# Kernel optimization log

Hardware: AMD Instinct MI355X
Metric: run time of the kernel (lower is better)

## Reference

```python
import jax, jax.numpy as jnp
import numpy as np

B, T, D = 8, 2048, 1024

def _ln(x, g, b, eps=1e-5):
    mu = x.mean(-1, keepdims=True)
    var = ((x - mu) ** 2).mean(-1, keepdims=True)
    return (x - mu) * jax.lax.rsqrt(var + eps) * g + b

def setup_inputs() -> dict:
    key = jax.random.key(0)
    ks = jax.random.split(key, 8)
    s = 1.0 / np.sqrt(D)
    return {
        "x": jax.random.normal(ks[0], (B, T, D), jnp.float32),
        "Wq": jax.random.normal(ks[1], (D, D), jnp.float32) * s,
        "bq": jnp.zeros((D,), jnp.float32),
        "Wk": jax.random.normal(ks[2], (D, D), jnp.float32) * s,
        "bk": jnp.zeros((D,), jnp.float32),
        "Wv": jax.random.normal(ks[3], (D, D), jnp.float32) * s,
        "bv": jnp.zeros((D,), jnp.float32),
        "pos_bias": jax.random.normal(ks[4], (T, T), jnp.float32) * 0.1,
        "ln1_g": jnp.ones((D,), jnp.float32),
        "ln1_b": jnp.zeros((D,), jnp.float32),
        "W1": jax.random.normal(ks[5], (D, 4 * D), jnp.float32) * s,
        "b1": jnp.zeros((4 * D,), jnp.float32),
        "W2": jax.random.normal(ks[6], (4 * D, D), jnp.float32) * (1.0 / np.sqrt(4 * D)),
        "b2": jnp.zeros((D,), jnp.float32),
        "ln2_g": jnp.ones((D,), jnp.float32),
        "ln2_b": jnp.zeros((D,), jnp.float32),
    }

def reference(x, Wq, bq, Wk, bk, Wv, bv, pos_bias, ln1_g, ln1_b,
              W1, b1, W2, b2, ln2_g, ln2_b):
    # --- pre-norm AFT-full attention + residual ---
    h = _ln(x, ln1_g, ln1_b)
    q = h @ Wq + bq                      # [B,T,D]
    k = h @ Wk + bk
    v = h @ Wv + bv
    # global-max stabilization (cancels in the ratio)
    ek = jnp.exp(k - jax.lax.stop_gradient(k.max()))
    ew = jnp.exp(pos_bias - jax.lax.stop_gradient(pos_bias.max()))  # [T,T]
    num = jnp.einsum('ts,bsd->btd', ew, ek * v)
    den = jnp.einsum('ts,bsd->btd', ew, ek)
    attn = jax.nn.sigmoid(q) * (num / den)
    x = attn + x
    # --- pre-norm MLP + residual ---
    h = _ln(x, ln2_g, ln2_b)
    h = jax.nn.relu(h @ W1 + b1) @ W2 + b2
    return h + x
```

## Files before the change

### kernel.cpp

```cpp
#include <hip/hip_runtime.h>
#include <hip/hip_bf16.h>
#include <stdint.h>

typedef __hip_bfloat16 bf16;
typedef __attribute__((ext_vector_type(4))) float f32x4;
typedef __attribute__((ext_vector_type(8))) short bf16x8;

#define BB   8
#define TT   2048
#define DD   1024
#define MM   (BB * TT)

enum { EPI_Q = 0, EPI_K, EPI_V, EPI_ND, EPI_MLP1, EPI_MLP2 };

static __device__ __forceinline__ void async_ld16(const bf16* g, bf16* l) {
  __builtin_amdgcn_global_load_lds(
      (const __attribute__((address_space(1))) void*)g,
      (__attribute__((address_space(3))) void*)l, 16, 0, 0);
}

template<int EPI>
__global__ __launch_bounds__(512, 2)
void gemm_bt(const bf16* __restrict__ A, const bf16* __restrict__ B,
             int M, int N, int K,
             long long strideAz, long long strideBz,
             float* __restrict__ Cf,
             bf16* __restrict__ Cb, long long strideCz,
             const float* __restrict__ bias,
             const float* __restrict__ add,
             bf16* __restrict__ ekv)
{
  (void)M;
  __shared__ __align__(16) bf16 lds[65536];

  const int tid  = threadIdx.x;
  const int wave = tid >> 6;
  const int lane = tid & 63;

  const int nwg = (int)gridDim.x;
  const int bid = (int)blockIdx.x;
  const int swz = (bid & 7) * (nwg >> 3) + (bid >> 3);
  int bn, bm, bz;
  if constexpr (EPI == EPI_ND) {
    bn = swz & 7; bm = (swz >> 3) & 7; bz = swz >> 6;
  } else {
    const int nbn = N >> 8;
    const int lnb = 31 - __clz(nbn);
    bn = swz & (nbn - 1); bm = swz >> lnb; bz = 0;
  }
  A += (size_t)bz * strideAz;
  B += (size_t)bz * strideBz;

  const int wm = (wave >> 2) * 128;
  const int wn = (wave & 3) * 64;

  const int lr = lane >> 2;
  const int lc = (((lane & 3) ^ ((lane >> 3) & 3))) * 8;
  const bf16* Ag0 = A + ((size_t)bm * 256 + wave * 32 + lr) * K + lc;
  const bf16* Bg0 = B + ((size_t)bn * 256 + wave * 32 + lr) * K + lc;
  const size_t K16 = (size_t)16 * K;
  const int ldsAW = wave * 1024;
  const int ldsBW = 32768 + wave * 1024;
  const int NT = K >> 5;

  auto stageA = [&](int tt) {
    const int bo = (tt & 3) * 8192;
    const bf16* g = Ag0 + (size_t)(tt & (NT - 1)) * 32;
    async_ld16(g,       &lds[bo + ldsAW]);
    async_ld16(g + K16, &lds[bo + ldsAW + 512]);
  };
  auto stageB = [&](int tt) {
    const int bo = (tt & 3) * 8192;
    const bf16* g = Bg0 + (size_t)(tt & (NT - 1)) * 32;
    async_ld16(g,       &lds[bo + ldsBW]);
    async_ld16(g + K16, &lds[bo + ldsBW + 512]);
  };

  f32x4 acc[8][4];
#pragma unroll
  for (int i = 0; i < 8; ++i)
#pragma unroll
    for (int j = 0; j < 4; ++j) acc[i][j] = {0.f, 0.f, 0.f, 0.f};

  stageA(0); stageB(0);
  stageA(1); stageB(1);
  stageA(2); stageB(2);
  __builtin_amdgcn_sched_barrier(0);
  asm volatile("s_waitcnt vmcnt(8)" ::: "memory");
  __builtin_amdgcn_s_barrier();
  __builtin_amdgcn_sched_barrier(0);

  const int fm32 = (lane & 15) * 32;
  const int qs = (((lane >> 4) ^ ((lane >> 1) & 3))) * 8;

  bf16x8 bfrP[4], bfrN[4], afA[4], afB[4];

  {
    const int ab0 = wm * 32 + fm32 + qs;
    const int bb0 = 32768 + wn * 32 + fm32 + qs;
#pragma unroll
    for (int j = 0; j < 4; ++j) bfrP[j] = *(const bf16x8*)&lds[bb0 + j * 512];
#pragma unroll
    for (int i = 0; i < 4; ++i) afA[i] = *(const bf16x8*)&lds[ab0 + i * 512];
  }
  __builtin_amdgcn_sched_barrier(0);

#define TILE_BODY(t, bfrC, bfrX)                                               \
  {                                                                            \
    const int ab  = ((t) & 3) * 8192 + wm * 32 + fm32 + qs;                    \
    const int abn = (((t) + 1) & 3) * 8192 + wm * 32 + fm32 + qs;              \
    const int bbn = 32768 + (((t) + 1) & 3) * 8192 + wn * 32 + fm32 + qs;      \
                                                        \
    _Pragma("unroll")                                                          \
    for (int i = 0; i < 4; ++i)                                                \
      afB[i] = *(const bf16x8*)&lds[ab + 2048 + i * 512];                      \
    stageA((t) + 3);                                                           \
    __builtin_amdgcn_sched_barrier(0);                                         \
    asm volatile("s_waitcnt vmcnt(6) lgkmcnt(4)" ::: "memory");                \
    __builtin_amdgcn_sched_barrier(0);                                         \
    __builtin_amdgcn_s_setprio(1);                                             \
    _Pragma("unroll")                                                          \
    for (int i = 0; i < 4; ++i)                                                \
      _Pragma("unroll")                                                        \
      for (int j = 0; j < 4; ++j)                                              \
        acc[i][j] = __builtin_amdgcn_mfma_f32_16x16x32_bf16(                   \
            afA[i], bfrC[j], acc[i][j], 0, 0, 0);                              \
    __builtin_amdgcn_s_setprio(0);                                             \
    __builtin_amdgcn_s_barrier();                                              \
    __builtin_amdgcn_sched_barrier(0);                                         \
                                                        \
    _Pragma("unroll")                                                          \
    for (int j = 0; j < 4; ++j)                                                \
      bfrX[j] = *(const bf16x8*)&lds[bbn + j * 512];                           \
    _Pragma("unroll")                                                          \
    for (int i = 0; i < 4; ++i)                                                \
      afA[i] = *(const bf16x8*)&lds[abn + i * 512];                            \
    stageB((t) + 3);                                                           \
    __builtin_amdgcn_sched_barrier(0);                                         \
    asm volatile("s_waitcnt lgkmcnt(8)" ::: "memory");                         \
    __builtin_amdgcn_sched_barrier(0);                                         \
    __builtin_amdgcn_s_setprio(1);                                             \
    _Pragma("unroll")                                                          \
    for (int i = 0; i < 4; ++i)                                                \
      _Pragma("unroll")                                                        \
      for (int j = 0; j < 4; ++j)                                              \
        acc[4 + i][j] = __builtin_amdgcn_mfma_f32_16x16x32_bf16(               \
            afB[i], bfrC[j], acc[4 + i][j], 0, 0, 0);                          \
    __builtin_amdgcn_s_setprio(0);                                             \
    __builtin_amdgcn_s_barrier();                                              \
    __builtin_amdgcn_sched_barrier(0);                                         \
  }

  for (int tp = 0; tp < NT; tp += 2) {
    TILE_BODY(tp,     bfrP, bfrN);
    TILE_BODY(tp + 1, bfrN, bfrP);
  }
#undef TILE_BODY

  const int cr = (lane >> 4) * 4;
  const int cc = lane & 15;
#pragma unroll
  for (int i = 0; i < 8; ++i) {
#pragma unroll
    for (int j = 0; j < 4; ++j) {
#pragma unroll
      for (int r = 0; r < 4; ++r) {
        const int gm = bm * 256 + wm + i * 16 + cr + r;
        const int gn = bn * 256 + wn + j * 16 + cc;
        float v = acc[i][j][r];
        if constexpr (EPI == EPI_Q) {
          v += bias[gn];
          Cb[(size_t)gm * N + gn] = __float2bfloat16(v);
        } else if constexpr (EPI == EPI_K) {
          v = __expf(v + bias[gm]);
          const int b = gn >> 11, t = gn & (TT - 1);
          ekv[((size_t)b << 22) + (size_t)(1024 + gm) * TT + t] =
              __float2bfloat16(v);
        } else if constexpr (EPI == EPI_V) {
          v += bias[gm];
          const int b = gn >> 11, t = gn & (TT - 1);
          const size_t base = ((size_t)b << 22);
          const float ek =
              __bfloat162float(ekv[base + (size_t)(1024 + gm) * TT + t]);
          ekv[base + (size_t)gm * TT + t] = __float2bfloat16(v * ek);
        } else if constexpr (EPI == EPI_ND) {
          Cb[(size_t)bz * strideCz + (size_t)gm * N + gn] =
              __float2bfloat16(v);
        } else if constexpr (EPI == EPI_MLP1) {
          v = fmaxf(v + bias[gn], 0.0f);
          Cb[(size_t)gm * N + gn] = __float2bfloat16(v);
        } else {
          v += bias[gn] + add[(size_t)gm * N + gn];
          Cf[(size_t)gm * N + gn] = v;
        }
      }
    }
  }
}

__global__ __launch_bounds__(256)
void transpose_cast(const float* __restrict__ W, bf16* __restrict__ Wt,
                    int K, int N)
{
  __shared__ float tile[32][33];
  const int n0 = blockIdx.x * 32, k0 = blockIdx.y * 32;
  const int tx = threadIdx.x, ty = threadIdx.y;
#pragma unroll
  for (int i = 0; i < 32; i += 8)
    tile[ty + i][tx] = W[(size_t)(k0 + ty + i) * N + n0 + tx];
  __syncthreads();
#pragma unroll
  for (int i = 0; i < 32; i += 8)
    Wt[(size_t)(n0 + ty + i) * K + k0 + tx] =
        __float2bfloat16(tile[tx][ty + i]);
}

__global__ __launch_bounds__(256)
void ew_kernel(const float* __restrict__ pb, bf16* __restrict__ ew)
{
  const size_t gid = (size_t)blockIdx.x * 256 + threadIdx.x;
  const float4 v = *(const float4*)(pb + gid * 4);
  union { bf16 h[4]; unsigned long long u; } pk;
  pk.h[0] = __float2bfloat16(__expf(v.x));
  pk.h[1] = __float2bfloat16(__expf(v.y));
  pk.h[2] = __float2bfloat16(__expf(v.z));
  pk.h[3] = __float2bfloat16(__expf(v.w));
  *(unsigned long long*)(ew + gid * 4) = pk.u;
}

__global__ __launch_bounds__(256)
void ln_kernel(const float* __restrict__ x, const float* __restrict__ g,
               const float* __restrict__ b, bf16* __restrict__ out)
{
  const int row = blockIdx.x;
  const int tid = threadIdx.x;
  const float4 v = ((const float4*)(x + (size_t)row * DD))[tid];
  float s  = v.x + v.y + v.z + v.w;
  float s2 = v.x * v.x + v.y * v.y + v.z * v.z + v.w * v.w;
#pragma unroll
  for (int o = 32; o; o >>= 1) {
    s  += __shfl_down(s, o);
    s2 += __shfl_down(s2, o);
  }
  __shared__ float red[8];
  if ((tid & 63) == 0) { red[tid >> 6] = s; red[4 + (tid >> 6)] = s2; }
  __syncthreads();
  const float ts  = red[0] + red[1] + red[2] + red[3];
  const float ts2 = red[4] + red[5] + red[6] + red[7];
  const float mu = ts * (1.0f / DD);
  const float rs = rsqrtf(ts2 * (1.0f / DD) - mu * mu + 1e-5f);
  const float4 gv = ((const float4*)g)[tid];
  const float4 bv = ((const float4*)b)[tid];
  union { bf16 h[4]; unsigned long long u; } pk;
  pk.h[0] = __float2bfloat16((v.x - mu) * rs * gv.x + bv.x);
  pk.h[1] = __float2bfloat16((v.y - mu) * rs * gv.y + bv.y);
  pk.h[2] = __float2bfloat16((v.z - mu) * rs * gv.z + bv.z);
  pk.h[3] = __float2bfloat16((v.w - mu) * rs * gv.w + bv.w);
  ((unsigned long long*)(out + (size_t)row * DD))[tid] = pk.u;
}

__global__ __launch_bounds__(256)
void combine_ln_kernel(const bf16* __restrict__ q, const bf16* __restrict__ nd,
                       const float* __restrict__ x,
                       const float* __restrict__ g, const float* __restrict__ b,
                       float* __restrict__ x2, bf16* __restrict__ hout)
{
  const int row = blockIdx.x;
  const int tid = threadIdx.x;
  const int c = tid * 4;
  const bf16* ndr = nd + (size_t)row * 2048;
  union { unsigned long long u; bf16 h[4]; } un, ud, uq;
  un.u = *(const unsigned long long*)(ndr + c);
  ud.u = *(const unsigned long long*)(ndr + 1024 + c);
  uq.u = *(const unsigned long long*)(q + (size_t)row * DD + c);
  const float4 xv = *(const float4*)(x + (size_t)row * DD + c);
  float4 o;
  o.x = xv.x + (__bfloat162float(un.h[0]) / __bfloat162float(ud.h[0])) /
                   (1.0f + __expf(-__bfloat162float(uq.h[0])));
  o.y = xv.y + (__bfloat162float(un.h[1]) / __bfloat162float(ud.h[1])) /
                   (1.0f + __expf(-__bfloat162float(uq.h[1])));
  o.z = xv.z + (__bfloat162float(un.h[2]) / __bfloat162float(ud.h[2])) /
                   (1.0f + __expf(-__bfloat162float(uq.h[2])));
  o.w = xv.w + (__bfloat162float(un.h[3]) / __bfloat162float(ud.h[3])) /
                   (1.0f + __expf(-__bfloat162float(uq.h[3])));
  *(float4*)(x2 + (size_t)row * DD + c) = o;

  float s  = o.x + o.y + o.z + o.w;
  float s2 = o.x * o.x + o.y * o.y + o.z * o.z + o.w * o.w;
#pragma unroll
  for (int off = 32; off; off >>= 1) {
    s  += __shfl_down(s, off);
    s2 += __shfl_down(s2, off);
  }
  __shared__ float red[8];
  if ((tid & 63) == 0) { red[tid >> 6] = s; red[4 + (tid >> 6)] = s2; }
  __syncthreads();
  const float ts  = red[0] + red[1] + red[2] + red[3];
  const float ts2 = red[4] + red[5] + red[6] + red[7];
  const float mu = ts * (1.0f / DD);
  const float rs = rsqrtf(ts2 * (1.0f / DD) - mu * mu + 1e-5f);
  const float4 gv = ((const float4*)g)[tid];
  const float4 bv = ((const float4*)b)[tid];
  union { bf16 h[4]; unsigned long long u; } pk;
  pk.h[0] = __float2bfloat16((o.x - mu) * rs * gv.x + bv.x);
  pk.h[1] = __float2bfloat16((o.y - mu) * rs * gv.y + bv.y);
  pk.h[2] = __float2bfloat16((o.z - mu) * rs * gv.z + bv.z);
  pk.h[3] = __float2bfloat16((o.w - mu) * rs * gv.w + bv.w);
  ((unsigned long long*)(hout + (size_t)row * DD))[tid] = pk.u;
}

extern "C" void kernel_launch(void* const* d_in, const int* in_sizes, int n_in,
                              void* d_out, int out_size, void* d_ws,
                              size_t ws_size, hipStream_t stream)
{
  (void)in_sizes; (void)n_in; (void)out_size; (void)ws_size;
  const float* x   = (const float*)d_in[0];
  const float* Wq  = (const float*)d_in[1];
  const float* bq  = (const float*)d_in[2];
  const float* Wk  = (const float*)d_in[3];
  const float* bk  = (const float*)d_in[4];
  const float* Wv  = (const float*)d_in[5];
  const float* bv  = (const float*)d_in[6];
  const float* pb  = (const float*)d_in[7];
  const float* g1  = (const float*)d_in[8];
  const float* be1 = (const float*)d_in[9];
  const float* W1  = (const float*)d_in[10];
  const float* bm1 = (const float*)d_in[11];
  const float* W2  = (const float*)d_in[12];
  const float* bm2 = (const float*)d_in[13];
  const float* g2  = (const float*)d_in[14];
  const float* be2 = (const float*)d_in[15];
  float* out = (float*)d_out;

  const size_t MiB = 1024 * 1024;
  char* w = (char*)d_ws;
  bf16* hbf = (bf16*)w;  w += (size_t)MM * DD * 2;
  bf16* wqt = (bf16*)w;  w += (size_t)DD * DD * 2;
  bf16* wkt = (bf16*)w;  w += (size_t)DD * DD * 2;
  bf16* wvt = (bf16*)w;  w += (size_t)DD * DD * 2;
  bf16* w1t = (bf16*)w;  w += (size_t)4096 * DD * 2;
  bf16* w2t = (bf16*)w;  w += (size_t)DD * 4096 * 2;
  char* scr = w;
  bf16* qbf = (bf16*)scr;
  bf16* ewb = (bf16*)(scr + 32 * MiB);
  bf16* ekv = (bf16*)(scr + 40 * MiB);
  bf16* nd  = (bf16*)(scr + 104 * MiB);
  bf16* mid = (bf16*)scr;
  float* x2 = out;

  const dim3 tb(32, 8);
  transpose_cast<<<dim3(DD / 32, DD / 32), tb, 0, stream>>>(Wq, wqt, DD, DD);
  transpose_cast<<<dim3(DD / 32, DD / 32), tb, 0, stream>>>(Wk, wkt, DD, DD);
  transpose_cast<<<dim3(DD / 32, DD / 32), tb, 0, stream>>>(Wv, wvt, DD, DD);
  transpose_cast<<<dim3(4096 / 32, DD / 32), tb, 0, stream>>>(W1, w1t, DD, 4096);
  transpose_cast<<<dim3(DD / 32, 4096 / 32), tb, 0, stream>>>(W2, w2t, 4096, DD);

  ew_kernel<<<(TT * TT / 4) / 256, 256, 0, stream>>>(pb, ewb);
  ln_kernel<<<MM, 256, 0, stream>>>(x, g1, be1, hbf);

  gemm_bt<EPI_Q><<<(MM / 256) * (DD / 256), 512, 0, stream>>>(
      hbf, wqt, MM, DD, DD, 0, 0, nullptr, qbf, 0, bq, nullptr, nullptr);
  gemm_bt<EPI_K><<<(DD / 256) * (MM / 256), 512, 0, stream>>>(
      wkt, hbf, DD, MM, DD, 0, 0, nullptr, nullptr, 0, bk, nullptr, ekv);
  gemm_bt<EPI_V><<<(DD / 256) * (MM / 256), 512, 0, stream>>>(
      wvt, hbf, DD, MM, DD, 0, 0, nullptr, nullptr, 0, bv, nullptr, ekv);
  gemm_bt<EPI_ND><<<BB * (TT / 256) * (TT / 256), 512, 0, stream>>>(
      ewb, ekv, TT, TT, TT, 0, (long long)TT * TT, nullptr, nd,
      (long long)TT * TT, nullptr, nullptr, nullptr);

  combine_ln_kernel<<<MM, 256, 0, stream>>>(qbf, nd, x, g2, be2, x2, hbf);

  gemm_bt<EPI_MLP1><<<(MM / 256) * (4096 / 256), 512, 0, stream>>>(
      hbf, w1t, MM, 4096, DD, 0, 0, nullptr, mid, 0, bm1, nullptr, nullptr);
  gemm_bt<EPI_MLP2><<<(MM / 256) * (DD / 256), 512, 0, stream>>>(
      mid, w2t, MM, DD, 4096, 0, 0, out, nullptr, 0, bm2, x2, nullptr);
}
```

Baseline: 732.0 us.

## Fuse K and V projections into one interleaved GEMM and merge small kernels

```diff
diff --git a/kernel.cpp b/kernel.cpp
--- a/kernel.cpp
+++ b/kernel.cpp
@@ -11,7 +11,7 @@
 #define DD   1024
 #define MM   (BB * TT)
 
-enum { EPI_Q = 0, EPI_K, EPI_V, EPI_ND, EPI_MLP1, EPI_MLP2 };
+enum { EPI_Q = 0, EPI_KV, EPI_ND, EPI_MLP1, EPI_MLP2 };
 
 static __device__ __forceinline__ void async_ld16(const bf16* g, bf16* l) {
   __builtin_amdgcn_global_load_lds(
@@ -171,18 +171,16 @@
         if constexpr (EPI == EPI_Q) {
           v += bias[gn];
           Cb[(size_t)gm * N + gn] = __float2bfloat16(v);
-        } else if constexpr (EPI == EPI_K) {
-          v = __expf(v + bias[gm]);
-          const int b = gn >> 11, t = gn & (TT - 1);
-          ekv[((size_t)b << 22) + (size_t)(1024 + gm) * TT + t] =
-              __float2bfloat16(v);
-        } else if constexpr (EPI == EPI_V) {
-          v += bias[gm];
-          const int b = gn >> 11, t = gn & (TT - 1);
-          const size_t base = ((size_t)b << 22);
-          const float ek =
-              __bfloat162float(ekv[base + (size_t)(1024 + gm) * TT + t]);
-          ekv[base + (size_t)gm * TT + t] = __float2bfloat16(v * ek);
+        } else if constexpr (EPI == EPI_KV) {
+          if ((r & 1) == 0) {
+            const int d = gm >> 1;
+            const float ek = __expf(acc[i][j][r] + bias[d]);
+            const float vv = acc[i][j][r + 1] + add[d];
+            const int b = gn >> 11, t = gn & (TT - 1);
+            const size_t base = ((size_t)b << 22);
+            ekv[base + (size_t)(1024 + d) * TT + t] = __float2bfloat16(ek);
+            ekv[base + (size_t)d * TT + t] = __float2bfloat16(ek * vv);
+          }
         } else if constexpr (EPI == EPI_ND) {
           Cb[(size_t)bz * strideCz + (size_t)gm * N + gn] =
               __float2bfloat16(v);
@@ -200,7 +198,7 @@
 
 __global__ __launch_bounds__(256)
 void transpose_cast(const float* __restrict__ W, bf16* __restrict__ Wt,
-                    int K, int N)
+                    int K, int N, int rs, int ro)
 {
   __shared__ float tile[32][33];
   const int n0 = blockIdx.x * 32, k0 = blockIdx.y * 32;
@@ -211,29 +209,52 @@
   __syncthreads();
 #pragma unroll
   for (int i = 0; i < 32; i += 8)
-    Wt[(size_t)(n0 + ty + i) * K + k0 + tx] =
+    Wt[((size_t)(n0 + ty + i) * rs + ro) * K + k0 + tx] =
         __float2bfloat16(tile[tx][ty + i]);
 }
 
 __global__ __launch_bounds__(256)
-void ew_kernel(const float* __restrict__ pb, bf16* __restrict__ ew)
-{
-  const size_t gid = (size_t)blockIdx.x * 256 + threadIdx.x;
-  const float4 v = *(const float4*)(pb + gid * 4);
-  union { bf16 h[4]; unsigned long long u; } pk;
-  pk.h[0] = __float2bfloat16(__expf(v.x));
-  pk.h[1] = __float2bfloat16(__expf(v.y));
-  pk.h[2] = __float2bfloat16(__expf(v.z));
-  pk.h[3] = __float2bfloat16(__expf(v.w));
-  *(unsigned long long*)(ew + gid * 4) = pk.u;
+void transpose3(const float* __restrict__ Wq, const float* __restrict__ Wk,
+                const float* __restrict__ Wv, bf16* __restrict__ wqt,
+                bf16* __restrict__ wkv)
+{
+  __shared__ float tile[32][33];
+  const int z = blockIdx.z;
+  const float* W = (z == 0) ? Wq : (z == 1) ? Wk : Wv;
+  bf16* Wt = (z == 0) ? wqt : wkv;
+  const int rs = (z == 0) ? 1 : 2;
+  const int ro = (z == 2) ? 1 : 0;
+  const int n0 = blockIdx.x * 32, k0 = blockIdx.y * 32;
+  const int tx = threadIdx.x, ty = threadIdx.y;
+#pragma unroll
+  for (int i = 0; i < 32; i += 8)
+    tile[ty + i][tx] = W[(size_t)(k0 + ty + i) * DD + n0 + tx];
+  __syncthreads();
+#pragma unroll
+  for (int i = 0; i < 32; i += 8)
+    Wt[((size_t)(n0 + ty + i) * rs + ro) * DD + k0 + tx] =
+        __float2bfloat16(tile[tx][ty + i]);
 }
 
 __global__ __launch_bounds__(256)
-void ln_kernel(const float* __restrict__ x, const float* __restrict__ g,
-               const float* __restrict__ b, bf16* __restrict__ out)
-{
-  const int row = blockIdx.x;
+void ln_ew_kernel(const float* __restrict__ x, const float* __restrict__ g,
+                  const float* __restrict__ b, bf16* __restrict__ out,
+                  const float* __restrict__ pb, bf16* __restrict__ ew)
+{
+  const int blk = blockIdx.x;
   const int tid = threadIdx.x;
+  if (blk >= MM) {
+    const size_t gid = (size_t)(blk - MM) * 256 + tid;
+    const float4 v = *(const float4*)(pb + gid * 4);
+    union { bf16 h[4]; unsigned long long u; } pk;
+    pk.h[0] = __float2bfloat16(__expf(v.x));
+    pk.h[1] = __float2bfloat16(__expf(v.y));
+    pk.h[2] = __float2bfloat16(__expf(v.z));
+    pk.h[3] = __float2bfloat16(__expf(v.w));
+    *(unsigned long long*)(ew + gid * 4) = pk.u;
+    return;
+  }
+  const int row = blk;
   const float4 v = ((const float4*)(x + (size_t)row * DD))[tid];
   float s  = v.x + v.y + v.z + v.w;
   float s2 = v.x * v.x + v.y * v.y + v.z * v.z + v.w * v.w;
@@ -336,8 +357,7 @@
   char* w = (char*)d_ws;
   bf16* hbf = (bf16*)w;  w += (size_t)MM * DD * 2;
   bf16* wqt = (bf16*)w;  w += (size_t)DD * DD * 2;
-  bf16* wkt = (bf16*)w;  w += (size_t)DD * DD * 2;
-  bf16* wvt = (bf16*)w;  w += (size_t)DD * DD * 2;
+  bf16* wkv = (bf16*)w;  w += (size_t)2 * DD * DD * 2;
   bf16* w1t = (bf16*)w;  w += (size_t)4096 * DD * 2;
   bf16* w2t = (bf16*)w;  w += (size_t)DD * 4096 * 2;
   char* scr = w;
@@ -349,21 +369,20 @@
   float* x2 = out;
 
   const dim3 tb(32, 8);
-  transpose_cast<<<dim3(DD / 32, DD / 32), tb, 0, stream>>>(Wq, wqt, DD, DD);
-  transpose_cast<<<dim3(DD / 32, DD / 32), tb, 0, stream>>>(Wk, wkt, DD, DD);
-  transpose_cast<<<dim3(DD / 32, DD / 32), tb, 0, stream>>>(Wv, wvt, DD, DD);
-  transpose_cast<<<dim3(4096 / 32, DD / 32), tb, 0, stream>>>(W1, w1t, DD, 4096);
-  transpose_cast<<<dim3(DD / 32, 4096 / 32), tb, 0, stream>>>(W2, w2t, 4096, DD);
-
-  ew_kernel<<<(TT * TT / 4) / 256, 256, 0, stream>>>(pb, ewb);
-  ln_kernel<<<MM, 256, 0, stream>>>(x, g1, be1, hbf);
+  transpose3<<<dim3(DD / 32, DD / 32, 3), tb, 0, stream>>>(Wq, Wk, Wv,
+                                                           wqt, wkv);
+  transpose_cast<<<dim3(4096 / 32, DD / 32), tb, 0, stream>>>(
+      W1, w1t, DD, 4096, 1, 0);
+  transpose_cast<<<dim3(DD / 32, 4096 / 32), tb, 0, stream>>>(
+      W2, w2t, 4096, DD, 1, 0);
+
+  ln_ew_kernel<<<MM + (TT * TT / 4) / 256, 256, 0, stream>>>(
+      x, g1, be1, hbf, pb, ewb);
 
   gemm_bt<EPI_Q><<<(MM / 256) * (DD / 256), 512, 0, stream>>>(
       hbf, wqt, MM, DD, DD, 0, 0, nullptr, qbf, 0, bq, nullptr, nullptr);
-  gemm_bt<EPI_K><<<(DD / 256) * (MM / 256), 512, 0, stream>>>(
-      wkt, hbf, DD, MM, DD, 0, 0, nullptr, nullptr, 0, bk, nullptr, ekv);
-  gemm_bt<EPI_V><<<(DD / 256) * (MM / 256), 512, 0, stream>>>(
-      wvt, hbf, DD, MM, DD, 0, 0, nullptr, nullptr, 0, bv, nullptr, ekv);
+  gemm_bt<EPI_KV><<<(2048 / 256) * (MM / 256), 512, 0, stream>>>(
+      wkv, hbf, 2048, MM, DD, 0, 0, nullptr, nullptr, 0, bk, bv, ekv);
   gemm_bt<EPI_ND><<<BB * (TT / 256) * (TT / 256), 512, 0, stream>>>(
       ewb, ekv, TT, TT, TT, 0, (long long)TT * TT, nullptr, nd,
       (long long)TT * TT, nullptr, nullptr, nullptr);
```

Measured after the change: 705.6 us. 1.04x faster.
